# Kernel tuning notes

Hardware: AMD Instinct MI355X
Metric: run time of the kernel (lower is better)

The kernel has to match this reference:

```python
import jax, jax.numpy as jnp
import numpy as np

H = 256  # hidden_units
B = 64   # batch
D = 2048 # question length


def setup_inputs() -> dict:
    key = jax.random.key(0)
    ks = jax.random.split(key, 9)
    s = 1.0 / np.sqrt(H)
    return {
        "context": jax.random.normal(ks[0], (B, H), dtype=jnp.float32),
        "question": jax.random.normal(ks[1], (B, D, H), dtype=jnp.float32),
        "hidden": jax.random.normal(ks[2], (1, B, H), dtype=jnp.float32),
        "W1": jax.random.uniform(ks[3], (H, H), jnp.float32, -s, s),  # linear_g1, no bias
        "W2": jax.random.uniform(ks[4], (H, H), jnp.float32, -s, s),  # linear_g2
        "b2": jax.random.uniform(ks[5], (H,), jnp.float32, -s, s),
        "W3": jax.random.uniform(ks[6], (H, H), jnp.float32, -s, s),  # linear_g3, no bias
        "W4": jax.random.uniform(ks[7], (1, H), jnp.float32, -s, s),  # linear_g4
        "b4": jax.random.uniform(ks[8], (1,), jnp.float32, -s, s),
    }


def reference(context, question, hidden, W1, W2, b2, W3, W4, b4):
    # hidden: (1,B,H) -> (B,1,H); linear_g3 (no bias)
    g3 = jnp.swapaxes(hidden, 0, 1) @ W3.T            # (B,1,H)
    # linear_g2 on context, then unsqueeze(1)
    g2 = (context @ W2.T + b2)[:, None, :]            # (B,1,H)
    # linear_g1 on question (no bias)
    g1 = question @ W1.T                              # (B,D,H)
    # The torch repeat/view sequence is exactly a broadcast add in (B,D,H)
    s = jnp.tanh(g2 + g3 + g1)                        # (B,D,H)
    scores = s @ W4.T + b4                            # (B,D,1)
    attn = jax.nn.softmax(scores, axis=1)             # softmax over D
    # attn.transpose(1,2) bmm question -> (B,1,H)
    return jnp.einsum('bdo,bdh->boh', attn, question)
```

## Files before the change

kernel.cpp:

```cpp
#include <hip/hip_runtime.h>
#include <hip/hip_bf16.h>
#include <math.h>

#define HD 256
#define BB 64
#define DD 2048
#define NQ 4
#define NST 8

typedef __attribute__((ext_vector_type(8))) short  short8;
typedef __attribute__((ext_vector_type(4))) float  float4v;
typedef __attribute__((ext_vector_type(4))) unsigned uint4v;
typedef __attribute__((ext_vector_type(4))) unsigned short ushort4v;

__device__ inline unsigned short f2bf(float f) {
    unsigned u = __builtin_bit_cast(unsigned, f);
    u += 0x7FFFu + ((u >> 16) & 1u);
    return (unsigned short)(u >> 16);
}

__device__ inline float fast_exp2(float x) {
    float r;
    asm("v_exp_f32 %0, %1" : "=v"(r) : "v"(x));
    return r;
}
__device__ inline float fast_expf(float x) { return fast_exp2(x * 1.4426950408889634f); }
__device__ inline float fast_tanh(float x) {
    float y = x * 2.8853900817779268f;
    y = fminf(fmaxf(y, -30.f), 30.f);
    float t = fast_exp2(y);
    float r;
    asm("v_rcp_f32 %0, %1" : "=v"(r) : "v"(t + 1.f));
    return (t - 1.f) * r;
}

#define SYNC_LDS() do { asm volatile("s_waitcnt lgkmcnt(0)" ::: "memory"); \
                        __builtin_amdgcn_s_barrier(); \
                        asm volatile("" ::: "memory"); } while (0)
#define WAITV8()  asm volatile("s_waitcnt vmcnt(8)" ::: "memory")
#define WAITV0()  asm volatile("s_waitcnt vmcnt(0)" ::: "memory")
#define BARRIER() do { __builtin_amdgcn_s_barrier(); asm volatile("" ::: "memory"); } while (0)

__device__ inline void load_lds16(const void* g, void* l) {
    __builtin_amdgcn_global_load_lds(
        (const __attribute__((address_space(1))) void*)g,
        (__attribute__((address_space(3))) void*)l, 16, 0, 0);
}

__device__ inline void stage(const float* qtile, float* buf, int wave, int lane) {
    const int half = lane & 1;
    #pragma unroll
    for (int i = 0; i < 8; ++i) {
        int r = wave * 8 + i;
        int gsrc = ((((lane >> 1) ^ (r & 7)) << 1) | half) << 4;
        load_lds16((const char*)qtile + (size_t)r * 1024 + gsrc,
                   (char*)buf + r * 1024);
    }
}

__global__ __launch_bounds__(256) void k_prep(const float* __restrict__ W1,
                                              unsigned short* __restrict__ w1b,
                                              const float* __restrict__ ctx,
                                              const float* __restrict__ hid,
                                              const float* __restrict__ W2,
                                              const float* __restrict__ b2,
                                              const float* __restrict__ W3,
                                              float* __restrict__ g23) {
    if (blockIdx.x < 64) {
        int i = blockIdx.x * 256 + threadIdx.x;
        float4v v = ((const float4v*)W1)[i];
        ushort4v o;
        o[0] = f2bf(v[0]); o[1] = f2bf(v[1]); o[2] = f2bf(v[2]); o[3] = f2bf(v[3]);
        ((ushort4v*)w1b)[i] = o;
    } else {
        int b = blockIdx.x - 64, t = threadIdx.x;
        __shared__ float c[HD], hh[HD];
        c[t]  = ctx[b * HD + t];
        hh[t] = hid[b * HD + t];
        __syncthreads();
        const float4v* w2 = (const float4v*)(W2 + (size_t)t * HD);
        const float4v* w3 = (const float4v*)(W3 + (size_t)t * HD);
        float acc = b2[t];
        #pragma unroll 8
        for (int k = 0; k < 64; ++k) {
            float4v a = w2[k], d = w3[k];
            int k4 = k * 4;
            acc += c[k4] * a[0] + c[k4 + 1] * a[1] + c[k4 + 2] * a[2] + c[k4 + 3] * a[3];
            acc += hh[k4] * d[0] + hh[k4 + 1] * d[1] + hh[k4 + 2] * d[2] + hh[k4 + 3] * d[3];
        }
        g23[b * HD + t] = acc;
    }
}

__global__ __launch_bounds__(512) void k_fused(const float* __restrict__ q,
                                               const unsigned short* __restrict__ w1b,
                                               const float* __restrict__ g23,
                                               const float* __restrict__ W4,
                                               float* __restrict__ pl,
                                               float* __restrict__ pO) {
    __shared__ __attribute__((aligned(16))) float buf0[64 * HD];
    __shared__ __attribute__((aligned(16))) float buf1[64 * HD];
    __shared__ float sp_t[4][64];

    const int t = threadIdx.x;
    const int chunk = blockIdx.x, b = blockIdx.y;
    const int lane = t & 63, wave = t >> 6;
    const int l15 = lane & 15, lk = lane >> 4;
    const int hg = wave >> 1, dh = wave & 1;
    const int hb = hg * 64;
    const int cq = lane & 7, ro = lane >> 3;

    const float* qc = q + ((size_t)b * DD + chunk * 512) * HD;

    stage(qc, buf0, wave, lane);

    short8 bfr[8][4];
    #pragma unroll
    for (int kb = 0; kb < 8; ++kb)
        #pragma unroll
        for (int nf = 0; nf < 4; ++nf)
            bfr[kb][nf] = *(const short8*)&w1b[(size_t)(hb + nf * 16 + l15) * HD + kb * 32 + lk * 8];

    float gv[4][4], wv[4][4];
    #pragma unroll
    for (int nf = 0; nf < 4; ++nf)
        #pragma unroll
        for (int r = 0; r < 4; ++r) {
            int h = hb + nf * 16 + lk * 4 + r;
            gv[nf][r] = g23[b * HD + h];
            wv[nf][r] = W4[h];
        }

    float l = 0.f;
    float4v O = {0.f, 0.f, 0.f, 0.f};
    float* cur = buf0;
    float* nxt = buf1;

    #pragma unroll 1
    for (int st = 0; st < NST; ++st) {
        SYNC_LDS();
        if (st + 1 < NST) {
            stage(qc + (size_t)(st + 1) * 64 * HD, nxt, wave, lane);
            WAITV8();
        } else {
            WAITV0();
        }
        BARRIER();

        float s0, s1;
        #pragma unroll
        for (int mf = 0; mf < 2; ++mf) {
            float4v a0 = {0.f,0.f,0.f,0.f}, a1 = {0.f,0.f,0.f,0.f};
            float4v a2 = {0.f,0.f,0.f,0.f}, a3 = {0.f,0.f,0.f,0.f};
            const int d = dh * 32 + mf * 16 + l15;
            const int dsw = d & 7;
            #pragma unroll
            for (int kb = 0; kb < 8; ++kb) {
                int g = kb * 4 + lk;
                int byte = d * 1024 + ((g ^ dsw) << 5);
                float4v lo = *(const float4v*)((const char*)cur + byte);
                float4v hi = *(const float4v*)((const char*)cur + byte + 16);
                short8 bq;
                {
                    uint4v u;
                    asm("v_cvt_pk_bf16_f32 %0, %1, %2" : "=v"(u[0]) : "v"(lo[0]), "v"(lo[1]));
                    asm("v_cvt_pk_bf16_f32 %0, %1, %2" : "=v"(u[1]) : "v"(lo[2]), "v"(lo[3]));
                    asm("v_cvt_pk_bf16_f32 %0, %1, %2" : "=v"(u[2]) : "v"(hi[0]), "v"(hi[1]));
                    asm("v_cvt_pk_bf16_f32 %0, %1, %2" : "=v"(u[3]) : "v"(hi[2]), "v"(hi[3]));
                    bq = __builtin_bit_cast(short8, u);
                }
                a0 = __builtin_amdgcn_mfma_f32_16x16x32_bf16(bfr[kb][0], bq, a0, 0, 0, 0);
                a1 = __builtin_amdgcn_mfma_f32_16x16x32_bf16(bfr[kb][1], bq, a1, 0, 0, 0);
                a2 = __builtin_amdgcn_mfma_f32_16x16x32_bf16(bfr[kb][2], bq, a2, 0, 0, 0);
                a3 = __builtin_amdgcn_mfma_f32_16x16x32_bf16(bfr[kb][3], bq, a3, 0, 0, 0);
            }
            float s = 0.f;
            #pragma unroll
            for (int r = 0; r < 4; ++r) s += fast_tanh(a0[r] + gv[0][r]) * wv[0][r];
            #pragma unroll
            for (int r = 0; r < 4; ++r) s += fast_tanh(a1[r] + gv[1][r]) * wv[1][r];
            #pragma unroll
            for (int r = 0; r < 4; ++r) s += fast_tanh(a2[r] + gv[2][r]) * wv[2][r];
            #pragma unroll
            for (int r = 0; r < 4; ++r) s += fast_tanh(a3[r] + gv[3][r]) * wv[3][r];
            s += __shfl_xor(s, 16, 64);
            s += __shfl_xor(s, 32, 64);
            if (mf == 0) s0 = s; else s1 = s;
        }
        float sv = (lane < 16) ? s0 : s1;
        if (lane < 32) sp_t[hg][dh * 32 + lane] = sv;
        SYNC_LDS();

        float sc = sp_t[0][lane] + sp_t[1][lane] + sp_t[2][lane] + sp_t[3][lane];
        float w = fast_exp2(sc * 1.4426950408889634f);
        l += w;
        const int gq = wave * 4 + (cq >> 1);
        const int hoff = (cq & 1) << 4;
        #pragma unroll
        for (int i = 0; i < 8; ++i) {
            int d = ro * 8 + i;
            float wd = __shfl(w, d, 64);
            int byte = d * 1024 + ((gq ^ (d & 7)) << 5) + hoff;
            float4v v = *(const float4v*)((const char*)cur + byte);
            O += wd * v;
        }

        float* tmp = cur; cur = nxt; nxt = tmp;
    }

    #pragma unroll
    for (int j = 0; j < 4; ++j) {
        O[j] += __shfl_xor(O[j], 8, 64);
        O[j] += __shfl_xor(O[j], 16, 64);
        O[j] += __shfl_xor(O[j], 32, 64);
    }
    if (ro == 0)
        *(float4v*)&pO[((size_t)(b * NQ + chunk)) * HD + wave * 32 + cq * 4] = O;

    l += __shfl_xor(l, 1, 64);
    l += __shfl_xor(l, 2, 64);
    l += __shfl_xor(l, 4, 64);
    l += __shfl_xor(l, 8, 64);
    l += __shfl_xor(l, 16, 64);
    l += __shfl_xor(l, 32, 64);
    if (t == 0) pl[b * NQ + chunk] = l;
}

__global__ __launch_bounds__(256) void k_comb(const float* __restrict__ pl,
                                              const float* __restrict__ pO,
                                              float* __restrict__ out) {
    int b = blockIdx.x, t = threadIdx.x;
    float L = pl[b * NQ] + pl[b * NQ + 1] + pl[b * NQ + 2] + pl[b * NQ + 3];
    float s = 0.f;
    #pragma unroll
    for (int c = 0; c < NQ; ++c) s += pO[((size_t)(b * NQ + c)) * HD + t];
    out[b * HD + t] = s / L;
}

extern "C" void kernel_launch(void* const* d_in, const int* in_sizes, int n_in,
                              void* d_out, int out_size, void* d_ws, size_t ws_size,
                              hipStream_t stream) {
    (void)in_sizes; (void)n_in; (void)out_size; (void)ws_size;
    const float* ctx = (const float*)d_in[0];
    const float* q   = (const float*)d_in[1];
    const float* hid = (const float*)d_in[2];
    const float* W1  = (const float*)d_in[3];
    const float* W2  = (const float*)d_in[4];
    const float* b2  = (const float*)d_in[5];
    const float* W3  = (const float*)d_in[6];
    const float* W4  = (const float*)d_in[7];
    float* out = (float*)d_out;

    char* ws = (char*)d_ws;
    unsigned short* w1b = (unsigned short*)(ws);
    float* g23 = (float*)(ws + 131072);
    float* pl  = (float*)(ws + 196608);
    float* pO  = (float*)(ws + 197632);

    k_prep <<<dim3(128), dim3(256), 0, stream>>>(W1, w1b, ctx, hid, W2, b2, W3, g23);
    k_fused<<<dim3(NQ, BB), dim3(512), 0, stream>>>(q, w1b, g23, W4, pl, pO);
    k_comb <<<dim3(BB), dim3(256), 0, stream>>>(pl, pO, out);
}
```

Before: 76.86 us.

## Repartition waves to split hidden dim eight ways across all rows

Each of the 8 waves now owns a 32-wide slice of the hidden dimension and processes all 64 question rows per stage. Previously the split was 4 hidden groups of 64 times 2 row halves. This halves the per-wave W1 fragment registers and accumulators, and the score reduction now sums 8 partial rows from shared memory. The cost is that each wave reads every staged row from LDS and converts it to bf16, so LDS reads and conversion instructions roughly double.

```diff
diff --git a/kernel.cpp b/kernel.cpp
--- a/kernel.cpp
+++ b/kernel.cpp
@@ -17,6 +17,15 @@
     unsigned u = __builtin_bit_cast(unsigned, f);
     u += 0x7FFFu + ((u >> 16) & 1u);
     return (unsigned short)(u >> 16);
+}
+
+__device__ inline short8 cvt8(float4v lo, float4v hi) {
+    uint4v u;
+    asm("v_cvt_pk_bf16_f32 %0, %1, %2" : "=v"(u[0]) : "v"(lo[0]), "v"(lo[1]));
+    asm("v_cvt_pk_bf16_f32 %0, %1, %2" : "=v"(u[1]) : "v"(lo[2]), "v"(lo[3]));
+    asm("v_cvt_pk_bf16_f32 %0, %1, %2" : "=v"(u[2]) : "v"(hi[0]), "v"(hi[1]));
+    asm("v_cvt_pk_bf16_f32 %0, %1, %2" : "=v"(u[3]) : "v"(hi[2]), "v"(hi[3]));
+    return __builtin_bit_cast(short8, u);
 }
 
 __device__ inline float fast_exp2(float x) {
@@ -100,30 +109,29 @@
                                                float* __restrict__ pO) {
     __shared__ __attribute__((aligned(16))) float buf0[64 * HD];
     __shared__ __attribute__((aligned(16))) float buf1[64 * HD];
-    __shared__ float sp_t[4][64];
+    __shared__ float sp[8][64];
 
     const int t = threadIdx.x;
-    const int chunk = blockIdx.x, b = blockIdx.y;
+    const int qtr = blockIdx.x, b = blockIdx.y;
     const int lane = t & 63, wave = t >> 6;
     const int l15 = lane & 15, lk = lane >> 4;
-    const int hg = wave >> 1, dh = wave & 1;
-    const int hb = hg * 64;
+    const int hb = wave * 32;
     const int cq = lane & 7, ro = lane >> 3;
 
-    const float* qc = q + ((size_t)b * DD + chunk * 512) * HD;
-
-    stage(qc, buf0, wave, lane);
-
-    short8 bfr[8][4];
+    const float* qq = q + ((size_t)b * DD + qtr * 512) * HD;
+
+    stage(qq, buf0, wave, lane);
+
+    short8 bfr[8][2];
     #pragma unroll
     for (int kb = 0; kb < 8; ++kb)
         #pragma unroll
-        for (int nf = 0; nf < 4; ++nf)
+        for (int nf = 0; nf < 2; ++nf)
             bfr[kb][nf] = *(const short8*)&w1b[(size_t)(hb + nf * 16 + l15) * HD + kb * 32 + lk * 8];
 
-    float gv[4][4], wv[4][4];
-    #pragma unroll
-    for (int nf = 0; nf < 4; ++nf)
+    float gv[2][4], wv[2][4];
+    #pragma unroll
+    for (int nf = 0; nf < 2; ++nf)
         #pragma unroll
         for (int r = 0; r < 4; ++r) {
             int h = hb + nf * 16 + lk * 4 + r;
@@ -140,19 +148,17 @@
     for (int st = 0; st < NST; ++st) {
         SYNC_LDS();
         if (st + 1 < NST) {
-            stage(qc + (size_t)(st + 1) * 64 * HD, nxt, wave, lane);
+            stage(qq + (size_t)(st + 1) * 64 * HD, nxt, wave, lane);
             WAITV8();
         } else {
             WAITV0();
         }
         BARRIER();
 
-        float s0, s1;
-        #pragma unroll
-        for (int mf = 0; mf < 2; ++mf) {
-            float4v a0 = {0.f,0.f,0.f,0.f}, a1 = {0.f,0.f,0.f,0.f};
-            float4v a2 = {0.f,0.f,0.f,0.f}, a3 = {0.f,0.f,0.f,0.f};
-            const int d = dh * 32 + mf * 16 + l15;
+        #pragma unroll
+        for (int mf = 0; mf < 4; ++mf) {
+            float4v acc0 = {0.f, 0.f, 0.f, 0.f}, acc1 = {0.f, 0.f, 0.f, 0.f};
+            const int d = mf * 16 + l15;
             const int dsw = d & 7;
             #pragma unroll
             for (int kb = 0; kb < 8; ++kb) {
@@ -160,38 +166,23 @@
                 int byte = d * 1024 + ((g ^ dsw) << 5);
                 float4v lo = *(const float4v*)((const char*)cur + byte);
                 float4v hi = *(const float4v*)((const char*)cur + byte + 16);
-                short8 bq;
-                {
-                    uint4v u;
-                    asm("v_cvt_pk_bf16_f32 %0, %1, %2" : "=v"(u[0]) : "v"(lo[0]), "v"(lo[1]));
-                    asm("v_cvt_pk_bf16_f32 %0, %1, %2" : "=v"(u[1]) : "v"(lo[2]), "v"(lo[3]));
-                    asm("v_cvt_pk_bf16_f32 %0, %1, %2" : "=v"(u[2]) : "v"(hi[0]), "v"(hi[1]));
-                    asm("v_cvt_pk_bf16_f32 %0, %1, %2" : "=v"(u[3]) : "v"(hi[2]), "v"(hi[3]));
-                    bq = __builtin_bit_cast(short8, u);
-                }
-                a0 = __builtin_amdgcn_mfma_f32_16x16x32_bf16(bfr[kb][0], bq, a0, 0, 0, 0);
-                a1 = __builtin_amdgcn_mfma_f32_16x16x32_bf16(bfr[kb][1], bq, a1, 0, 0, 0);
-                a2 = __builtin_amdgcn_mfma_f32_16x16x32_bf16(bfr[kb][2], bq, a2, 0, 0, 0);
-                a3 = __builtin_amdgcn_mfma_f32_16x16x32_bf16(bfr[kb][3], bq, a3, 0, 0, 0);
+                short8 bq = cvt8(lo, hi);
+                acc0 = __builtin_amdgcn_mfma_f32_16x16x32_bf16(bfr[kb][0], bq, acc0, 0, 0, 0);
+                acc1 = __builtin_amdgcn_mfma_f32_16x16x32_bf16(bfr[kb][1], bq, acc1, 0, 0, 0);
             }
             float s = 0.f;
             #pragma unroll
-            for (int r = 0; r < 4; ++r) s += fast_tanh(a0[r] + gv[0][r]) * wv[0][r];
+            for (int r = 0; r < 4; ++r) s += fast_tanh(acc0[r] + gv[0][r]) * wv[0][r];
             #pragma unroll
-            for (int r = 0; r < 4; ++r) s += fast_tanh(a1[r] + gv[1][r]) * wv[1][r];
-            #pragma unroll
-            for (int r = 0; r < 4; ++r) s += fast_tanh(a2[r] + gv[2][r]) * wv[2][r];
-            #pragma unroll
-            for (int r = 0; r < 4; ++r) s += fast_tanh(a3[r] + gv[3][r]) * wv[3][r];
+            for (int r = 0; r < 4; ++r) s += fast_tanh(acc1[r] + gv[1][r]) * wv[1][r];
             s += __shfl_xor(s, 16, 64);
             s += __shfl_xor(s, 32, 64);
-            if (mf == 0) s0 = s; else s1 = s;
-        }
-        float sv = (lane < 16) ? s0 : s1;
-        if (lane < 32) sp_t[hg][dh * 32 + lane] = sv;
+            if (lk == 0) sp[wave][mf * 16 + l15] = s;
+        }
         SYNC_LDS();
 
-        float sc = sp_t[0][lane] + sp_t[1][lane] + sp_t[2][lane] + sp_t[3][lane];
+        float sc = sp[0][lane] + sp[1][lane] + sp[2][lane] + sp[3][lane]
+                 + sp[4][lane] + sp[5][lane] + sp[6][lane] + sp[7][lane];
         float w = fast_exp2(sc * 1.4426950408889634f);
         l += w;
         const int gq = wave * 4 + (cq >> 1);
@@ -215,7 +206,7 @@
         O[j] += __shfl_xor(O[j], 32, 64);
     }
     if (ro == 0)
-        *(float4v*)&pO[((size_t)(b * NQ + chunk)) * HD + wave * 32 + cq * 4] = O;
+        *(float4v*)&pO[((size_t)(b * NQ + qtr)) * HD + wave * 32 + cq * 4] = O;
 
     l += __shfl_xor(l, 1, 64);
     l += __shfl_xor(l, 2, 64);
@@ -223,7 +214,7 @@
     l += __shfl_xor(l, 8, 64);
     l += __shfl_xor(l, 16, 64);
     l += __shfl_xor(l, 32, 64);
-    if (t == 0) pl[b * NQ + chunk] = l;
+    if (t == 0) pl[b * NQ + qtr] = l;
 }
 
 __global__ __launch_bounds__(256) void k_comb(const float* __restrict__ pl,
```

New measurement: 68.21 us. 1.13x faster.
